# Optimization experiments

Hardware: AMD Instinct MI355X
Metric: run time of the kernel (lower is better)

## Reference

```python
import jax, jax.numpy as jnp
import numpy as np

N = 30        # samples per bezier curve
W = 60        # output image side
LENGTH = 160  # curves per sample
ALPHA = 2e-4  # gaussian splat bandwidth
VIEWBOX = (0.0, 0.0, 1.0, 1.0)
BATCH = 128


def _bezier_T(n):
    # matches the torch buffer: reparametrized t, then (reordered) Bernstein basis
    t = jnp.arange(n, dtype=jnp.float32) / n
    t = 2.0 * t**3 - 3.0 * t**2 + 2.0 * t
    t3 = t**3
    return jnp.stack([t3,
                      3.0 * (t**2 - t3),
                      3.0 * (t3 - 2.0 * t**2 + t),
                      (1.0 - t)**3], axis=1)  # [n, 4]


def setup_inputs() -> dict:
    key = jax.random.key(0)
    x = jax.random.uniform(key, (BATCH, LENGTH, 8), dtype=jnp.float32)
    return {"x": x}


def reference(x):
    B = x.shape[0]
    T = _bezier_T(N)                                   # [n, 4]
    board = jnp.arange(W, dtype=jnp.float32) / W       # [W]
    bX = board * VIEWBOX[2] + VIEWBOX[0]
    bY = board * VIEWBOX[3] + VIEWBOX[1]

    ctrl = x.reshape(B, LENGTH, 4, 2)
    pts = jnp.einsum('nk,blkc->blnc', T, ctrl)         # [B, L, n, 2] bezier samples
    X = pts[..., 0]                                    # [B, L, n]
    Y = pts[..., 1]

    # gaussian splat of each sampled point onto the pixel grid (separable)
    gX = jnp.exp(-jnp.square(bX[None, None, :, None] - X[:, :, None, :]) / ALPHA)  # [B, L, W, n]
    gY = jnp.exp(-jnp.square(bY[None, None, :, None] - Y[:, :, None, :]) / ALPHA)  # [B, L, W, n]

    # outer-product over the two axes, reduced over samples n and curves L
    res = jnp.einsum('blwn,blvn->bwv', gX, gY)         # [B, W, W]
    return jnp.minimum(res, 1.0)
```

## Files before the change

### kernel.cpp

```cpp
#include <hip/hip_runtime.h>


namespace {
constexpr int   kN = 30;
constexpr int   kW = 60;
constexpr int   kL = 160;
constexpr int   kB = 128;
constexpr float kAlphaInv = 5000.0f;
constexpr float kRadPix = 3.5f;
constexpr int   KSPLIT = 4;
constexpr int   CPB = kL / KSPLIT;
constexpr int   KPC = 32;
constexpr int   KBLK = CPB * KPC;
constexpr int   KC = 128;
constexpr int   NCH = KBLK / KC;
constexpr int   LDK = KC + 8;
constexpr int   kPix = kW * kW;
}

using f32x4 = __attribute__((ext_vector_type(4))) float;
using f16x8 = __attribute__((ext_vector_type(8))) _Float16;

__global__ __launch_bounds__(256, 2) void bezier_gemm_kernel(const float* __restrict__ x,
                                                             float* __restrict__ partial) {
  __shared__ _Float16 sh[2][64][LDK];
  const int b   = blockIdx.x / KSPLIT;
  const int ks  = blockIdx.x % KSPLIT;
  const int tid = threadIdx.x;
  const int lane = tid & 63;
  const int wid  = tid >> 6;
  const int wi = wid >> 1;
  const int vi = wid & 1;
  const int l15 = lane & 15;
  const int l4  = lane >> 4;

  f32x4 acc4[2][2] = {};

  const float* xb = x + ((size_t)b * kL + (size_t)ks * CPB) * 8;

  {
    uint4* shv = (uint4*)&sh[0][0][0];
    constexpr int NZ = 2 * 64 * LDK * 2 / 16;
    for (int i = tid; i < NZ; i += 256) shv[i] = make_uint4(0, 0, 0, 0);
  }

  const int col = tid & 127;
  const int mat = tid >> 7;
  const int n   = col & (KPC - 1);
  const bool valid = (n < kN);
  float B0, B1, B2, B3;
  {
    float t0 = (float)n * (1.0f / 30.0f);
    float t  = 2.0f * t0 * t0 * t0 - 3.0f * t0 * t0 + 2.0f * t0;
    float t2 = t * t, t3 = t2 * t;
    B0 = t3;
    B1 = 3.0f * (t2 - t3);
    B2 = 3.0f * (t3 - 2.0f * t2 + t);
    float omt = 1.0f - t;
    B3 = omt * omt * omt;
  }
  int lo_prev = 0;

  __syncthreads();

  for (int ch = 0; ch < NCH; ++ch) {
    if (valid) {
      const int lc = ch * 4 + (col >> 5);
      const float4* c = (const float4*)(xb + lc * 8);
      float4 c0 = c[0], c1 = c[1];
      float P = mat ? (B0 * c0.y + B1 * c0.w + B2 * c1.y + B3 * c1.w)
                    : (B0 * c0.x + B1 * c0.z + B2 * c1.x + B3 * c1.z);
      float fp = P * (float)kW;
      int lo = (int)ceilf(fp - kRadPix);
#pragma unroll
      for (int i = 0; i < 8; ++i) {
        int m = lo_prev + i;
        if (m >= 0 && m < kW) sh[mat][m][col] = (_Float16)0.0f;
      }
#pragma unroll
      for (int i = 0; i < 8; ++i) {
        int m = lo + i;
        float d = (float)m * (1.0f / 60.0f) - P;
        float e = __expf(-d * d * kAlphaInv);
        if (m >= 0 && m < kW) sh[mat][m][col] = (_Float16)e;
      }
      lo_prev = lo;
    }
    __syncthreads();

#pragma unroll
    for (int kk = 0; kk < KC; kk += 32) {
      const int ke = kk + l4 * 8;
      f16x8 a0 = *(const f16x8*)&sh[0][wi * 32 + l15][ke];
      f16x8 a1 = *(const f16x8*)&sh[0][wi * 32 + 16 + l15][ke];
      f16x8 b0 = *(const f16x8*)&sh[1][vi * 32 + l15][ke];
      f16x8 b1 = *(const f16x8*)&sh[1][vi * 32 + 16 + l15][ke];
      acc4[0][0] = __builtin_amdgcn_mfma_f32_16x16x32_f16(a0, b0, acc4[0][0], 0, 0, 0);
      acc4[0][1] = __builtin_amdgcn_mfma_f32_16x16x32_f16(a0, b1, acc4[0][1], 0, 0, 0);
      acc4[1][0] = __builtin_amdgcn_mfma_f32_16x16x32_f16(a1, b0, acc4[1][0], 0, 0, 0);
      acc4[1][1] = __builtin_amdgcn_mfma_f32_16x16x32_f16(a1, b1, acc4[1][1], 0, 0, 0);
    }
    __syncthreads();
  }

  float* pb = partial + (size_t)blockIdx.x * kPix;
#pragma unroll
  for (int mt = 0; mt < 2; ++mt) {
#pragma unroll
    for (int vt = 0; vt < 2; ++vt) {
      const int v = vi * 32 + vt * 16 + l15;
#pragma unroll
      for (int r = 0; r < 4; ++r) {
        const int w = wi * 32 + mt * 16 + l4 * 4 + r;
        if (w < kW && v < kW) pb[w * kW + v] = acc4[mt][vt][r];
      }
    }
  }
}

__global__ __launch_bounds__(256) void reduce_kernel(const float* __restrict__ partial,
                                                     float* __restrict__ out) {
  int i = blockIdx.x * 256 + threadIdx.x;
  if (i >= kB * kPix) return;
  int b = i / kPix;
  int j = i - b * kPix;
  const float* p = partial + (size_t)b * KSPLIT * kPix + j;
  float s = p[0] + p[kPix] + p[2 * kPix] + p[3 * kPix];
  out[i] = fminf(s, 1.0f);
}

__global__ __launch_bounds__(1024) void splat_direct_kernel(const float* __restrict__ x,
                                                            float* __restrict__ out) {
  __shared__ float res[kPix];
  const int b = blockIdx.x;
  const int tid = threadIdx.x;
  for (int i = tid; i < kPix; i += 1024) res[i] = 0.0f;
  __syncthreads();
  const float* xb = x + (size_t)b * kL * 8;
  for (int p = tid; p < kL * kN; p += 1024) {
    int l = p / kN;
    int n = p - l * kN;
    float t0 = (float)n * (1.0f / 30.0f);
    float t  = 2.0f * t0 * t0 * t0 - 3.0f * t0 * t0 + 2.0f * t0;
    float t2 = t * t, t3 = t2 * t;
    float B0 = t3, B1 = 3.0f * (t2 - t3), B2 = 3.0f * (t3 - 2.0f * t2 + t);
    float omt = 1.0f - t, B3 = omt * omt * omt;
    const float4* c = (const float4*)(xb + l * 8);
    float4 c0 = c[0], c1 = c[1];
    float X = B0 * c0.x + B1 * c0.z + B2 * c1.x + B3 * c1.z;
    float Y = B0 * c0.y + B1 * c0.w + B2 * c1.y + B3 * c1.w;
    float fx = X * kW, fy = Y * kW;
    int wlo = (int)ceilf(fx - kRadPix), vlo = (int)ceilf(fy - kRadPix);
    for (int i = 0; i < 8; ++i) {
      int w = wlo + i;
      if (w < 0 || w >= kW) continue;
      float dw = ((float)w - fx) * (1.0f / kW);
      float gx = __expf(-dw * dw * kAlphaInv);
      for (int j = 0; j < 8; ++j) {
        int v = vlo + j;
        if (v < 0 || v >= kW) continue;
        float dv = ((float)v - fy) * (1.0f / kW);
        atomicAdd(&res[w * kW + v], gx * __expf(-dv * dv * kAlphaInv));
      }
    }
  }
  __syncthreads();
  float* outb = out + (size_t)b * kPix;
  for (int i = tid; i < kPix; i += 1024) outb[i] = fminf(res[i], 1.0f);
}

extern "C" void kernel_launch(void* const* d_in, const int* in_sizes, int n_in,
                              void* d_out, int out_size, void* d_ws, size_t ws_size,
                              hipStream_t stream) {
  const float* x = (const float*)d_in[0];
  float* out = (float*)d_out;
  const size_t part_bytes = (size_t)kB * KSPLIT * kPix * sizeof(float);

  if (ws_size >= part_bytes) {
    float* partial = (float*)d_ws;
    bezier_gemm_kernel<<<dim3(kB * KSPLIT), dim3(256), 0, stream>>>(x, partial);
    int n = kB * kPix;
    reduce_kernel<<<dim3((n + 255) / 256), dim3(256), 0, stream>>>(partial, out);
  } else {
    splat_direct_kernel<<<dim3(kB), dim3(1024), 0, stream>>>(x, out);
  }
}
```

Baseline: 23.97 us.

## Double K-split, prefetch control points, and vectorize the partial reduction

Raises the split-K factor from 4 to 8, giving 1024 GEMM blocks that each handle 20 curves, and raises the occupancy hint to 4 blocks per CU. It also prefetches the next chunk's control points into registers so global load latency overlaps the current chunk's work, and moves the exp inside the bounds check. The reduce kernel now reads and writes float4 and sums over KSPLIT partials. The trade-off is twice the partial-buffer traffic and workspace size, and the reduce pass gets heavier, in exchange for more parallelism in the GEMM stage.

```diff
diff --git a/kernel.cpp b/kernel.cpp
--- a/kernel.cpp
+++ b/kernel.cpp
@@ -8,12 +8,10 @@
 constexpr int   kB = 128;
 constexpr float kAlphaInv = 5000.0f;
 constexpr float kRadPix = 3.5f;
-constexpr int   KSPLIT = 4;
+constexpr int   KSPLIT = 8;
 constexpr int   CPB = kL / KSPLIT;
-constexpr int   KPC = 32;
-constexpr int   KBLK = CPB * KPC;
 constexpr int   KC = 128;
-constexpr int   NCH = KBLK / KC;
+constexpr int   NCH = CPB * 32 / KC;
 constexpr int   LDK = KC + 8;
 constexpr int   kPix = kW * kW;
 }
@@ -21,12 +19,12 @@
 using f32x4 = __attribute__((ext_vector_type(4))) float;
 using f16x8 = __attribute__((ext_vector_type(8))) _Float16;
 
-__global__ __launch_bounds__(256, 2) void bezier_gemm_kernel(const float* __restrict__ x,
+__global__ __launch_bounds__(256, 4) void bezier_gemm_kernel(const float* __restrict__ x,
                                                              float* __restrict__ partial) {
   __shared__ _Float16 sh[2][64][LDK];
-  const int b   = blockIdx.x / KSPLIT;
-  const int ks  = blockIdx.x % KSPLIT;
-  const int tid = threadIdx.x;
+  const int b    = blockIdx.x / KSPLIT;
+  const int ks   = blockIdx.x % KSPLIT;
+  const int tid  = threadIdx.x;
   const int lane = tid & 63;
   const int wid  = tid >> 6;
   const int wi = wid >> 1;
@@ -46,7 +44,7 @@
 
   const int col = tid & 127;
   const int mat = tid >> 7;
-  const int n   = col & (KPC - 1);
+  const int n   = col & 31;
   const bool valid = (n < kN);
   float B0, B1, B2, B3;
   {
@@ -61,15 +59,22 @@
   }
   int lo_prev = 0;
 
+  const float4* cp = (const float4*)(xb + (col >> 5) * 8);
+  float4 pc0 = cp[0], pc1 = cp[1];
+
   __syncthreads();
 
   for (int ch = 0; ch < NCH; ++ch) {
+    float4 nc0, nc1;
+    if (ch + 1 < NCH) {
+      const float4* np = (const float4*)(xb + ((ch + 1) * 4 + (col >> 5)) * 8);
+      nc0 = np[0];
+      nc1 = np[1];
+    }
+
     if (valid) {
-      const int lc = ch * 4 + (col >> 5);
-      const float4* c = (const float4*)(xb + lc * 8);
-      float4 c0 = c[0], c1 = c[1];
-      float P = mat ? (B0 * c0.y + B1 * c0.w + B2 * c1.y + B3 * c1.w)
-                    : (B0 * c0.x + B1 * c0.z + B2 * c1.x + B3 * c1.z);
+      float P = mat ? (B0 * pc0.y + B1 * pc0.w + B2 * pc1.y + B3 * pc1.w)
+                    : (B0 * pc0.x + B1 * pc0.z + B2 * pc1.x + B3 * pc1.z);
       float fp = P * (float)kW;
       int lo = (int)ceilf(fp - kRadPix);
 #pragma unroll
@@ -80,9 +85,10 @@
 #pragma unroll
       for (int i = 0; i < 8; ++i) {
         int m = lo + i;
-        float d = (float)m * (1.0f / 60.0f) - P;
-        float e = __expf(-d * d * kAlphaInv);
-        if (m >= 0 && m < kW) sh[mat][m][col] = (_Float16)e;
+        if (m >= 0 && m < kW) {
+          float d = (float)m * (1.0f / 60.0f) - P;
+          sh[mat][m][col] = (_Float16)__expf(-d * d * kAlphaInv);
+        }
       }
       lo_prev = lo;
     }
@@ -101,6 +107,9 @@
       acc4[1][1] = __builtin_amdgcn_mfma_f32_16x16x32_f16(a1, b1, acc4[1][1], 0, 0, 0);
     }
     __syncthreads();
+
+    pc0 = nc0;
+    pc1 = nc1;
   }
 
   float* pb = partial + (size_t)blockIdx.x * kPix;
@@ -120,13 +129,24 @@
 
 __global__ __launch_bounds__(256) void reduce_kernel(const float* __restrict__ partial,
                                                      float* __restrict__ out) {
+  constexpr int F4 = kPix / 4;
   int i = blockIdx.x * 256 + threadIdx.x;
-  if (i >= kB * kPix) return;
-  int b = i / kPix;
-  int j = i - b * kPix;
-  const float* p = partial + (size_t)b * KSPLIT * kPix + j;
-  float s = p[0] + p[kPix] + p[2 * kPix] + p[3 * kPix];
-  out[i] = fminf(s, 1.0f);
+  if (i >= kB * F4) return;
+  int b = i / F4;
+  int j = i - b * F4;
+  const float4* p = (const float4*)partial + (size_t)b * KSPLIT * F4 + j;
+  float4 s = p[0];
+#pragma unroll
+  for (int k = 1; k < KSPLIT; ++k) {
+    float4 t = p[(size_t)k * F4];
+    s.x += t.x; s.y += t.y; s.z += t.z; s.w += t.w;
+  }
+  float4 r;
+  r.x = fminf(s.x, 1.0f);
+  r.y = fminf(s.y, 1.0f);
+  r.z = fminf(s.z, 1.0f);
+  r.w = fminf(s.w, 1.0f);
+  ((float4*)out)[i] = r;
 }
 
 __global__ __launch_bounds__(1024) void splat_direct_kernel(const float* __restrict__ x,
@@ -179,8 +199,8 @@
   if (ws_size >= part_bytes) {
     float* partial = (float*)d_ws;
     bezier_gemm_kernel<<<dim3(kB * KSPLIT), dim3(256), 0, stream>>>(x, partial);
-    int n = kB * kPix;
-    reduce_kernel<<<dim3((n + 255) / 256), dim3(256), 0, stream>>>(partial, out);
+    int n4 = kB * kPix / 4;
+    reduce_kernel<<<dim3((n4 + 255) / 256), dim3(256), 0, stream>>>(partial, out);
   } else {
     splat_direct_kernel<<<dim3(kB), dim3(1024), 0, stream>>>(x, out);
   }
```

New measurement: 25.51 us. +6.4%, slower.
